# Kernel optimization log

Hardware: AMD Instinct MI355X
Metric: run time of the kernel (lower is better)

## Reference

```python
import jax, jax.numpy as jnp
import numpy as np

B, I, D = 512, 128, 64


def setup_inputs() -> dict:
    key = jax.random.key(0)
    embeddings = jax.random.normal(key, (B, I, D), dtype=jnp.float32)
    return {"embeddings": embeddings}


def reference(embeddings):
    # Original: em_ij[b,i,j,d] = emb[b,i,d]*emb[b,j,d]; ctx = mean over j.
    # Algebraically: ctx[b,i,d] = emb[b,i,d] * mean_j emb[b,j,d] -- linear time,
    # no [B,I,I,D] materialization.
    mean_emb = jnp.mean(embeddings, axis=1, keepdims=True)  # [B,1,D]
    ctx_vec = embeddings * mean_emb                         # [B,I,D]
    # activation_function (undefined in the snippet; repo uses a smooth
    # pointwise activation -- tanh assumed). Dropout is identity in eval mode.
    return jnp.tanh(ctx_vec)
```

## Files before the change

kernel.cpp:

```cpp
#include <hip/hip_runtime.h>


#define BB 512
#define II 128
#define DD 64
#define ELEMS_PER_BATCH (II * DD)
#define VEC_PER_BATCH   (ELEMS_PER_BATCH / 4)
#define BLOCK 1024

typedef float vf4 __attribute__((ext_vector_type(4)));

__device__ __forceinline__ float fast_tanh(float x) {
    float e = __expf(2.0f * x);
    return __fmaf_rn(-2.0f, __builtin_amdgcn_rcpf(e + 1.0f), 1.0f);
}

__global__ __launch_bounds__(BLOCK) void ctx_tanh_kernel(
        const float* __restrict__ emb, float* __restrict__ out) {
    __shared__ vf4 s_part[BLOCK];
    __shared__ vf4 s_mean[16];

    const int b = blockIdx.x;
    const int t = threadIdx.x;
    const vf4* __restrict__ gin  = (const vf4*)(emb + (size_t)b * ELEMS_PER_BATCH);
    vf4* __restrict__       gout = (vf4*)(out + (size_t)b * ELEMS_PER_BATCH);

    vf4 v0 = __builtin_nontemporal_load(&gin[t]);
    vf4 v1 = __builtin_nontemporal_load(&gin[t + BLOCK]);

    s_part[t] = v0 + v1;
    __syncthreads();

    if (t < 256) {
        s_part[t] = s_part[t] + s_part[t + 256] + s_part[t + 512] + s_part[t + 768];
    }
    __syncthreads();

    if (t < 16) {
        vf4 s = (vf4)(0.0f);
        #pragma unroll
        for (int m = 0; m < 16; ++m) s += s_part[t + 16 * m];
        s_mean[t] = s * (1.0f / (float)II);
    }
    __syncthreads();

    const vf4 m = s_mean[t & 15];
    vf4 p0 = v0 * m, p1 = v1 * m;
    vf4 o0, o1;
    o0.x = fast_tanh(p0.x); o0.y = fast_tanh(p0.y);
    o0.z = fast_tanh(p0.z); o0.w = fast_tanh(p0.w);
    o1.x = fast_tanh(p1.x); o1.y = fast_tanh(p1.y);
    o1.z = fast_tanh(p1.z); o1.w = fast_tanh(p1.w);
    __builtin_nontemporal_store(o0, &gout[t]);
    __builtin_nontemporal_store(o1, &gout[t + BLOCK]);
}

extern "C" void kernel_launch(void* const* d_in, const int* in_sizes, int n_in,
                              void* d_out, int out_size, void* d_ws, size_t ws_size,
                              hipStream_t stream) {
    const float* emb = (const float*)d_in[0];
    float* out = (float*)d_out;
    ctx_tanh_kernel<<<dim3(BB), dim3(BLOCK), 0, stream>>>(emb, out);
}
```

Measured before the change: 69.74 us.

## Use 256-thread blocks with 8 vectors per thread and wave-shuffle reduction

Shrinks each block from 1024 to 256 threads, so every thread loads eight float4 vectors and sums them in registers. The column reduction now uses cross-lane xor shuffles within each 64-lane wave before a small shared-memory combine, replacing the large shared-memory tree with its extra barrier. The aim is fewer LDS round trips and barriers with more memory-level parallelism per thread. The cost is higher register pressure and fewer threads per block to hide memory latency.

```diff
diff --git a/kernel.cpp b/kernel.cpp
--- a/kernel.cpp
+++ b/kernel.cpp
@@ -6,7 +6,8 @@
 #define DD 64
 #define ELEMS_PER_BATCH (II * DD)
 #define VEC_PER_BATCH   (ELEMS_PER_BATCH / 4)
-#define BLOCK 1024
+#define BLOCK 256
+#define VPT (VEC_PER_BATCH / BLOCK)
 
 typedef float vf4 __attribute__((ext_vector_type(4)));
 
@@ -15,44 +16,56 @@
     return __fmaf_rn(-2.0f, __builtin_amdgcn_rcpf(e + 1.0f), 1.0f);
 }
 
+__device__ __forceinline__ vf4 shfl_xor_vf4(vf4 v, int mask) {
+    vf4 r;
+    r.x = __shfl_xor(v.x, mask, 64);
+    r.y = __shfl_xor(v.y, mask, 64);
+    r.z = __shfl_xor(v.z, mask, 64);
+    r.w = __shfl_xor(v.w, mask, 64);
+    return r;
+}
+
 __global__ __launch_bounds__(BLOCK) void ctx_tanh_kernel(
         const float* __restrict__ emb, float* __restrict__ out) {
-    __shared__ vf4 s_part[BLOCK];
+    __shared__ vf4 s_wpart[64];
     __shared__ vf4 s_mean[16];
 
     const int b = blockIdx.x;
     const int t = threadIdx.x;
+    const int lane = t & 63;
+    const int wave = t >> 6;
     const vf4* __restrict__ gin  = (const vf4*)(emb + (size_t)b * ELEMS_PER_BATCH);
     vf4* __restrict__       gout = (vf4*)(out + (size_t)b * ELEMS_PER_BATCH);
 
-    vf4 v0 = __builtin_nontemporal_load(&gin[t]);
-    vf4 v1 = __builtin_nontemporal_load(&gin[t + BLOCK]);
+    vf4 v[VPT];
+    #pragma unroll
+    for (int k = 0; k < VPT; ++k)
+        v[k] = __builtin_nontemporal_load(&gin[t + BLOCK * k]);
 
-    s_part[t] = v0 + v1;
-    __syncthreads();
+    vf4 acc = v[0];
+    #pragma unroll
+    for (int k = 1; k < VPT; ++k) acc += v[k];
 
-    if (t < 256) {
-        s_part[t] = s_part[t] + s_part[t + 256] + s_part[t + 512] + s_part[t + 768];
-    }
+    acc += shfl_xor_vf4(acc, 16);
+    acc += shfl_xor_vf4(acc, 32);
+    if (lane < 16) s_wpart[wave * 16 + lane] = acc;
     __syncthreads();
 
     if (t < 16) {
-        vf4 s = (vf4)(0.0f);
-        #pragma unroll
-        for (int m = 0; m < 16; ++m) s += s_part[t + 16 * m];
+        vf4 s = s_wpart[t] + s_wpart[t + 16] + s_wpart[t + 32] + s_wpart[t + 48];
         s_mean[t] = s * (1.0f / (float)II);
     }
     __syncthreads();
 
     const vf4 m = s_mean[t & 15];
-    vf4 p0 = v0 * m, p1 = v1 * m;
-    vf4 o0, o1;
-    o0.x = fast_tanh(p0.x); o0.y = fast_tanh(p0.y);
-    o0.z = fast_tanh(p0.z); o0.w = fast_tanh(p0.w);
-    o1.x = fast_tanh(p1.x); o1.y = fast_tanh(p1.y);
-    o1.z = fast_tanh(p1.z); o1.w = fast_tanh(p1.w);
-    __builtin_nontemporal_store(o0, &gout[t]);
-    __builtin_nontemporal_store(o1, &gout[t + BLOCK]);
+    #pragma unroll
+    for (int k = 0; k < VPT; ++k) {
+        vf4 p = v[k] * m;
+        vf4 o;
+        o.x = fast_tanh(p.x); o.y = fast_tanh(p.y);
+        o.z = fast_tanh(p.z); o.w = fast_tanh(p.w);
+        __builtin_nontemporal_store(o, &gout[t + BLOCK * k]);
+    }
 }
 
 extern "C" void kernel_launch(void* const* d_in, const int* in_sizes, int n_in,
```

New measurement: 68.78 us. Within noise of the previous version (-1.4%).
